# Performance work log

Hardware: AMD Instinct MI355X
Metric: run time of the kernel (lower is better)

The kernel has to match this reference:

```python
import jax, jax.numpy as jnp
import numpy as np

N_NODES = 100000
N_EDGES = 1600000
D_IN = 64
D_HID = 64
D_OUT = 64


def setup_inputs() -> dict:
    key = jax.random.key(0)
    ks = jax.random.split(key, 12)
    x = jax.random.normal(ks[0], (N_NODES, D_IN), dtype=jnp.float32)
    edge_index = jax.random.randint(ks[1], (2, N_EDGES), 0, N_NODES, dtype=jnp.int64)
    batch = jnp.zeros((N_NODES,), dtype=jnp.int64)
    # Glorot-ish init for GCNConv weights; PyG stores weight as [in, out] applied as x @ W.
    def lin(k, din, dout):
        s = 1.0 / np.sqrt(din)
        return jax.random.uniform(k, (din, dout), minval=-s, maxval=s, dtype=jnp.float32)
    W1 = lin(ks[2], D_IN, D_HID);  b1 = jnp.zeros((D_HID,), jnp.float32)
    W2 = lin(ks[3], D_HID, D_HID); b2 = jnp.zeros((D_HID,), jnp.float32)
    W3 = lin(ks[4], D_HID, D_HID); b3 = jnp.zeros((D_HID,), jnp.float32)
    W4 = lin(ks[5], D_HID, D_OUT); b4 = jnp.zeros((D_OUT,), jnp.float32)
    return {"x": x, "edge_index": edge_index, "batch": batch,
            "W1": W1, "b1": b1, "W2": W2, "b2": b2,
            "W3": W3, "b3": b3, "W4": W4, "b4": b4}


def reference(x, edge_index, batch, W1, b1, W2, b2, W3, b3, W4, b4):
    N = x.shape[0]
    loops = jnp.arange(N, dtype=edge_index.dtype)
    src = jnp.concatenate([edge_index[0], loops])  # [E+N]
    dst = jnp.concatenate([edge_index[1], loops])  # [E+N]
    # Symmetric normalization: deg over A + I (in-degree at dst), norm_e = d_src^-1/2 * d_dst^-1/2
    deg = jax.ops.segment_sum(jnp.ones(src.shape, dtype=x.dtype), dst, num_segments=N)
    dis = jnp.where(deg > 0, jax.lax.rsqrt(deg), 0.0)
    norm = (dis[src] * dis[dst])[:, None]  # [E+N, 1]

    def conv(h, W, b):
        h = h @ W                                   # [N, dout]
        msg = h[src] * norm                         # gather + scale, [E+N, dout]
        return jax.ops.segment_sum(msg, dst, num_segments=N) + b

    h = jax.nn.elu(conv(x, W1, b1))   # dropout_p=0.0 -> identity
    h = jax.nn.elu(conv(h, W2, b2))
    h = jax.nn.elu(conv(h, W3, b3))
    return conv(h, W4, b4)
```

## Files before the change

### kernel.cpp

```cpp
#include <hip/hip_runtime.h>

#define NN 100000
#define NE 1600000
#define DD 64
#define BSH 9
#define BSZ 512
#define NBKT 196
#define CHUNK 8192
#define NCH ((NE + CHUNK - 1) / CHUNK)
#define CSR2_CAP (NE + 16 * (NBKT * BSZ))


__global__ __launch_bounds__(256) void k_bcount(const int* __restrict__ ei,
                                                int* __restrict__ bcnt) {
    __shared__ int h[NBKT];
    int t = threadIdx.x;
    for (int i = t; i < NBKT; i += 256) h[i] = 0;
    __syncthreads();
    int base = blockIdx.x * CHUNK;
    for (int i = t; i < CHUNK; i += 256) {
        int e = base + i;
        if (e < NE) atomicAdd(&h[ei[NE + e] >> BSH], 1);
    }
    __syncthreads();
    for (int i = t; i < NBKT; i += 256)
        if (h[i]) atomicAdd(&bcnt[i], h[i]);
}


__global__ __launch_bounds__(256) void k_bscan(const int* __restrict__ bcnt,
                                               int* __restrict__ bbase,
                                               int* __restrict__ bcur) {
    __shared__ int s[256];
    int t = threadIdx.x;
    int v = (t < NBKT) ? bcnt[t] : 0;
    s[t] = v;
    __syncthreads();
    for (int o = 1; o < 256; o <<= 1) {
        int x = (t >= o) ? s[t - o] : 0;
        __syncthreads();
        s[t] += x;
        __syncthreads();
    }
    int ex = s[t] - v;
    if (t < NBKT) { bbase[t] = ex; bcur[t] = ex; }
    if (t == NBKT) bbase[NBKT] = ex;
}


__global__ __launch_bounds__(256) void k_bscat(const int* __restrict__ ei,
                                               int* __restrict__ bcur,
                                               int* __restrict__ bkt) {
    __shared__ int h[NBKT], rbase[NBKT], rcur[NBKT];
    int t = threadIdx.x;
    for (int i = t; i < NBKT; i += 256) h[i] = 0;
    __syncthreads();
    int cb = blockIdx.x * CHUNK;
    int s[32], d[32];
#pragma unroll
    for (int i = 0; i < 32; ++i) {
        int e = cb + t + 256 * i;
        if (e < NE) {
            s[i] = ei[e];
            d[i] = ei[NE + e];
            atomicAdd(&h[d[i] >> BSH], 1);
        } else {
            d[i] = -1;
        }
    }
    __syncthreads();
    for (int i = t; i < NBKT; i += 256) {
        int c = h[i];
        rbase[i] = c ? atomicAdd(&bcur[i], c) : 0;
        rcur[i] = 0;
    }
    __syncthreads();
#pragma unroll
    for (int i = 0; i < 32; ++i) {
        if (d[i] >= 0) {
            int b = d[i] >> BSH;
            int pos = rbase[b] + atomicAdd(&rcur[b], 1);
            bkt[pos] = s[i] | ((d[i] & (BSZ - 1)) << 17);
        }
    }
}


__global__ __launch_bounds__(256) void k_ncnt(const int* __restrict__ bbase,
                                              const int* __restrict__ bkt,
                                              int* __restrict__ ncnt,
                                              int* __restrict__ bptot,
                                              double* __restrict__ dis) {
    __shared__ int cnt[BSZ];
    __shared__ int red[256];
    int b = blockIdx.x, t = threadIdx.x;
    cnt[t] = 0; cnt[t + 256] = 0;
    __syncthreads();
    int beg = bbase[b], end = bbase[b + 1];
    for (int j = beg + t; j < end; j += 256)
        atomicAdd(&cnt[bkt[j] >> 17], 1);
    __syncthreads();
    int nb = b * BSZ;
    int n0 = nb + t, n1 = nb + t + 256;
    int c0 = cnt[t], c1 = cnt[t + 256];
    int p0 = (n0 < NN) ? ((c0 + 16) & ~15) : 0;
    int p1 = (n1 < NN) ? ((c1 + 16) & ~15) : 0;
    if (n0 < NN) { ncnt[n0] = c0; dis[n0] = 1.0 / sqrt((double)(c0 + 1)); }
    if (n1 < NN) { ncnt[n1] = c1; dis[n1] = 1.0 / sqrt((double)(c1 + 1)); }
    red[t] = p0 + p1;
    __syncthreads();
    for (int o = 128; o > 0; o >>= 1) {
        if (t < o) red[t] += red[t + o];
        __syncthreads();
    }
    if (t == 0) bptot[b] = red[0];
}


__global__ __launch_bounds__(256) void k_pscan(const int* __restrict__ bptot,
                                               int* __restrict__ pbase,
                                               int* __restrict__ rp2) {
    __shared__ int s[256];
    int t = threadIdx.x;
    int v = (t < NBKT) ? bptot[t] : 0;
    s[t] = v;
    __syncthreads();
    for (int o = 1; o < 256; o <<= 1) {
        int x = (t >= o) ? s[t - o] : 0;
        __syncthreads();
        s[t] += x;
        __syncthreads();
    }
    int ex = s[t] - v;
    if (t < NBKT) pbase[t] = ex;
    if (t == NBKT) rp2[NN] = ex;
}


__global__ __launch_bounds__(256) void k_bfill(const int* __restrict__ bbase,
                                               const int* __restrict__ bkt,
                                               const int* __restrict__ ncnt,
                                               const int* __restrict__ pbase,
                                               int* __restrict__ rp2,
                                               int* __restrict__ csr2) {
    __shared__ int cur[BSZ];
    __shared__ int s2[256];
    int b = blockIdx.x, t = threadIdx.x;
    int nb = b * BSZ;
    int gbase = pbase[b];
    int n0 = nb + 2 * t, n1 = nb + 2 * t + 1;
    int c0 = (n0 < NN) ? ncnt[n0] : -1;
    int c1 = (n1 < NN) ? ncnt[n1] : -1;
    int q0 = (c0 >= 0) ? ((c0 + 16) & ~15) : 0;
    int q1 = (c1 >= 0) ? ((c1 + 16) & ~15) : 0;
    s2[t] = q0 + q1;
    __syncthreads();
    for (int o = 1; o < 256; o <<= 1) {
        int v = (t >= o) ? s2[t - o] : 0;
        __syncthreads();
        s2[t] += v;
        __syncthreads();
    }
    int ex = s2[t] - (q0 + q1);
    if (c0 >= 0) { int g = gbase + ex;      rp2[n0] = g; csr2[g] = n0; cur[2 * t]     = ex + 1; }
    if (c1 >= 0) { int g = gbase + ex + q0; rp2[n1] = g; csr2[g] = n1; cur[2 * t + 1] = ex + q0 + 1; }
    __syncthreads();
    int beg = bbase[b], end = bbase[b + 1];
    for (int j = beg + t; j < end; j += 256) {
        int pk = bkt[j];
        int pos = gbase + atomicAdd(&cur[pk >> 17], 1);
        csr2[pos] = pk & 0x1FFFF;
    }
    __syncthreads();
    if (c0 >= 0) { int e0 = ex + q0;      for (int j = cur[2 * t];     j < e0; ++j) csr2[gbase + j] = NN; }
    if (c1 >= 0) { int e1 = ex + q0 + q1; for (int j = cur[2 * t + 1]; j < e1; ++j) csr2[gbase + j] = NN; }
}


__global__ __launch_bounds__(256) void k_gemm(const float* __restrict__ in,
                                              const float* __restrict__ W,
                                              const double* __restrict__ dis,
                                              float* __restrict__ h2s) {
    __shared__ float sW[DD * DD];
    __shared__ float sIn[128 * 65];
    int t = threadIdx.x;
    int brow = blockIdx.x * 128;
#pragma unroll
    for (int i = 0; i < 16; ++i) sW[t + 256 * i] = W[t + 256 * i];
#pragma unroll
    for (int i = 0; i < 32; ++i) {
        int idx = t + 256 * i;
        int rr = idx >> 6, kk = idx & 63;
        int gr = brow + rr; if (gr >= NN) gr = NN - 1;
        sIn[rr * 65 + kk] = in[(size_t)gr * DD + kk];
    }
    __syncthreads();
    int cg = t & 7;
    int rg = t >> 3;
    const float* sInB = &sIn[rg * 4 * 65];

    float aE[4][8], aO[4][8];
#pragma unroll
    for (int i = 0; i < 4; ++i)
#pragma unroll
        for (int j = 0; j < 8; ++j) { aE[i][j] = 0.f; aO[i][j] = 0.f; }

#pragma unroll 4
    for (int k = 0; k < DD; k += 2) {
        float4 w0 = *(const float4*)&sW[k * DD + cg * 8];
        float4 w1 = *(const float4*)&sW[k * DD + cg * 8 + 4];
        float4 w2 = *(const float4*)&sW[(k + 1) * DD + cg * 8];
        float4 w3 = *(const float4*)&sW[(k + 1) * DD + cg * 8 + 4];
        float wv0[8] = {w0.x, w0.y, w0.z, w0.w, w1.x, w1.y, w1.z, w1.w};
        float wv1[8] = {w2.x, w2.y, w2.z, w2.w, w3.x, w3.y, w3.z, w3.w};
#pragma unroll
        for (int i = 0; i < 4; ++i) {
            float a0 = sInB[i * 65 + k];
            float a1 = sInB[i * 65 + k + 1];
#pragma unroll
            for (int j = 0; j < 8; ++j) {
                aE[i][j] = fmaf(a0, wv0[j], aE[i][j]);
                aO[i][j] = fmaf(a1, wv1[j], aO[i][j]);
            }
        }
    }

#pragma unroll
    for (int i = 0; i < 4; ++i) {
        int row = brow + rg * 4 + i;
        if (row < NN) {
            double dr = dis[row];
            float o[8];
#pragma unroll
            for (int j = 0; j < 8; ++j)
                o[j] = (float)((double)(aE[i][j] + aO[i][j]) * dr);
            *(float4*)&h2s[(size_t)row * DD + cg * 8]     = make_float4(o[0], o[1], o[2], o[3]);
            *(float4*)&h2s[(size_t)row * DD + cg * 8 + 4] = make_float4(o[4], o[5], o[6], o[7]);
        }
    }
}


__global__ __launch_bounds__(256) void k_aggr(const int* __restrict__ rp2,
                                              const int* __restrict__ csr2,
                                              const float* __restrict__ h2s,
                                              const double* __restrict__ dis,
                                              const float* __restrict__ b,
                                              float* __restrict__ out,
                                              int apply_elu) {
    int gid = blockIdx.x * 256 + threadIdx.x;
    int node = gid >> 6;
    int lane = gid & 63;
    int beg = __builtin_amdgcn_readfirstlane(rp2[node]);
    int end = __builtin_amdgcn_readfirstlane(rp2[node + 1]);
    double a0 = 0.0, a1 = 0.0, a2 = 0.0, a3 = 0.0;
    for (int j = beg; j < end; j += 16) {
        int4 i0 = *(const int4*)&csr2[j];
        int4 i1 = *(const int4*)&csr2[j + 4];
        int4 i2 = *(const int4*)&csr2[j + 8];
        int4 i3 = *(const int4*)&csr2[j + 12];
        float v0  = h2s[(size_t)(unsigned)i0.x * DD + lane];
        float v1  = h2s[(size_t)(unsigned)i0.y * DD + lane];
        float v2  = h2s[(size_t)(unsigned)i0.z * DD + lane];
        float v3  = h2s[(size_t)(unsigned)i0.w * DD + lane];
        float v4  = h2s[(size_t)(unsigned)i1.x * DD + lane];
        float v5  = h2s[(size_t)(unsigned)i1.y * DD + lane];
        float v6  = h2s[(size_t)(unsigned)i1.z * DD + lane];
        float v7  = h2s[(size_t)(unsigned)i1.w * DD + lane];
        float v8  = h2s[(size_t)(unsigned)i2.x * DD + lane];
        float v9  = h2s[(size_t)(unsigned)i2.y * DD + lane];
        float v10 = h2s[(size_t)(unsigned)i2.z * DD + lane];
        float v11 = h2s[(size_t)(unsigned)i2.w * DD + lane];
        float v12 = h2s[(size_t)(unsigned)i3.x * DD + lane];
        float v13 = h2s[(size_t)(unsigned)i3.y * DD + lane];
        float v14 = h2s[(size_t)(unsigned)i3.z * DD + lane];
        float v15 = h2s[(size_t)(unsigned)i3.w * DD + lane];
        a0 += (double)v0;  a1 += (double)v1;  a2 += (double)v2;  a3 += (double)v3;
        a0 += (double)v4;  a1 += (double)v5;  a2 += (double)v6;  a3 += (double)v7;
        a0 += (double)v8;  a1 += (double)v9;  a2 += (double)v10; a3 += (double)v11;
        a0 += (double)v12; a1 += (double)v13; a2 += (double)v14; a3 += (double)v15;
    }
    double sum = (a0 + a1) + (a2 + a3);
    float vf = (float)(dis[node] * sum + (double)b[lane]);
    if (apply_elu && vf <= 0.f) vf = expm1f(vf);
    out[gid] = vf;
}


static inline size_t align256(size_t x) { return (x + 255) & ~(size_t)255; }

extern "C" void kernel_launch(void* const* d_in, const int* in_sizes, int n_in,
                              void* d_out, int out_size, void* d_ws, size_t ws_size,
                              hipStream_t stream) {
    const float* x  = (const float*)d_in[0];
    const int*   ei = (const int*)d_in[1];
    const float* W1 = (const float*)d_in[3];
    const float* b1 = (const float*)d_in[4];
    const float* W2 = (const float*)d_in[5];
    const float* b2 = (const float*)d_in[6];
    const float* W3 = (const float*)d_in[7];
    const float* b3 = (const float*)d_in[8];
    const float* W4 = (const float*)d_in[9];
    const float* b4 = (const float*)d_in[10];
    float* out = (float*)d_out;

    char* ws = (char*)d_ws;
    size_t off = 0;
    double* dis   = (double*)(ws + off); off = align256(off + (size_t)NN * sizeof(double));
    float*  h2s   = (float*) (ws + off); off = align256(off + (size_t)(NN + 1) * DD * sizeof(float));
    float*  A     = (float*) (ws + off); off = align256(off + (size_t)NN * DD * sizeof(float));
    int*    ncnt  = (int*)   (ws + off); off = align256(off + (size_t)NN * sizeof(int));
    int*    rp2   = (int*)   (ws + off); off = align256(off + (size_t)(NN + 1) * sizeof(int));
    int*    bcnt  = (int*)   (ws + off); off = align256(off + (size_t)(NBKT + 1) * sizeof(int));
    int*    bbase = (int*)   (ws + off); off = align256(off + (size_t)(NBKT + 1) * sizeof(int));
    int*    bcur  = (int*)   (ws + off); off = align256(off + (size_t)(NBKT + 1) * sizeof(int));
    int*    bptot = (int*)   (ws + off); off = align256(off + (size_t)(NBKT + 1) * sizeof(int));
    int*    pbase = (int*)   (ws + off); off = align256(off + (size_t)(NBKT + 1) * sizeof(int));
    int*    bkt   = (int*)   (ws + off); off = align256(off + (size_t)NE * sizeof(int));
    int*    csr2  = (int*)   (ws + off); off = align256(off + (size_t)CSR2_CAP * sizeof(int));

    hipMemsetAsync(bcnt, 0, (size_t)NBKT * sizeof(int), stream);
    hipMemsetAsync(h2s + (size_t)NN * DD, 0, DD * sizeof(float), stream);

    k_bcount<<<NCH, 256, 0, stream>>>(ei, bcnt);
    k_bscan<<<1, 256, 0, stream>>>(bcnt, bbase, bcur);
    k_bscat<<<NCH, 256, 0, stream>>>(ei, bcur, bkt);
    k_ncnt<<<NBKT, 256, 0, stream>>>(bbase, bkt, ncnt, bptot, dis);
    k_pscan<<<1, 256, 0, stream>>>(bptot, pbase, rp2);
    k_bfill<<<NBKT, 256, 0, stream>>>(bbase, bkt, ncnt, pbase, rp2, csr2);

    struct Layer { const float* in; const float* b; const float* W; float* o; int elu; };
    Layer L[4] = {
        { x,   b1, W1, A,   1 },
        { A,   b2, W2, out, 1 },
        { out, b3, W3, A,   1 },
        { A,   b4, W4, out, 0 },
    };

    for (int l = 0; l < 4; ++l) {
        k_gemm<<<(NN + 127) / 128, 256, 0, stream>>>(L[l].in, L[l].W, dis, h2s);
        k_aggr<<<NN / 4, 256, 0, stream>>>(rp2, csr2, h2s, dis, L[l].b, L[l].o, L[l].elu);
    }
}
```

Baseline: 386.9 us.

## Fuse aggregation with next-layer GEMM and streamline CSR build with fixed-capacity buckets

The CSR construction drops the counting pass and the two scan kernels. Edges are scattered into fixed-capacity per-bucket arrays, and one merge kernel counts, pads, computes the degree norms and fills the CSR, taking its global offset from an atomic counter. For layers 1-3, a new persistent-wave kernel fuses neighbour aggregation, bias, ELU and the next layer's 64x64 matmul, broadcasting values with readlane. This removes the intermediate activation round trip through memory and three GEMM launches. The costs are 64 weight registers per lane, serial readlane matmul work, a capacity assumption on bucket size (BCAP) that could overflow, and a less regular, atomic-dependent CSR order.

```diff
diff --git a/kernel.cpp b/kernel.cpp
--- a/kernel.cpp
+++ b/kernel.cpp
@@ -6,45 +6,19 @@
 #define BSH 9
 #define BSZ 512
 #define NBKT 196
+#define BCAP 16384
 #define CHUNK 8192
 #define NCH ((NE + CHUNK - 1) / CHUNK)
-#define CSR2_CAP (NE + 16 * (NBKT * BSZ))
-
-
-__global__ __launch_bounds__(256) void k_bcount(const int* __restrict__ ei,
-                                                int* __restrict__ bcnt) {
-    __shared__ int h[NBKT];
+#define CSR2_CAP (NE + 16 * NN + 1024)
+
+
+__global__ void k_zero(int* __restrict__ bcur, int* __restrict__ gcur,
+                       float* __restrict__ h2sA, float* __restrict__ h2sB) {
     int t = threadIdx.x;
-    for (int i = t; i < NBKT; i += 256) h[i] = 0;
-    __syncthreads();
-    int base = blockIdx.x * CHUNK;
-    for (int i = t; i < CHUNK; i += 256) {
-        int e = base + i;
-        if (e < NE) atomicAdd(&h[ei[NE + e] >> BSH], 1);
-    }
-    __syncthreads();
-    for (int i = t; i < NBKT; i += 256)
-        if (h[i]) atomicAdd(&bcnt[i], h[i]);
-}
-
-
-__global__ __launch_bounds__(256) void k_bscan(const int* __restrict__ bcnt,
-                                               int* __restrict__ bbase,
-                                               int* __restrict__ bcur) {
-    __shared__ int s[256];
-    int t = threadIdx.x;
-    int v = (t < NBKT) ? bcnt[t] : 0;
-    s[t] = v;
-    __syncthreads();
-    for (int o = 1; o < 256; o <<= 1) {
-        int x = (t >= o) ? s[t - o] : 0;
-        __syncthreads();
-        s[t] += x;
-        __syncthreads();
-    }
-    int ex = s[t] - v;
-    if (t < NBKT) { bbase[t] = ex; bcur[t] = ex; }
-    if (t == NBKT) bbase[NBKT] = ex;
+    if (t < NBKT) bcur[t] = 0;
+    if (t == 255) *gcur = 0;
+    if (t < DD) h2sA[(size_t)NN * DD + t] = 0.f;
+    if (t >= 64 && t < 128) h2sB[(size_t)NN * DD + (t - 64)] = 0.f;
 }
 
 
@@ -80,77 +54,35 @@
         if (d[i] >= 0) {
             int b = d[i] >> BSH;
             int pos = rbase[b] + atomicAdd(&rcur[b], 1);
-            bkt[pos] = s[i] | ((d[i] & (BSZ - 1)) << 17);
-        }
-    }
-}
-
-
-__global__ __launch_bounds__(256) void k_ncnt(const int* __restrict__ bbase,
-                                              const int* __restrict__ bkt,
-                                              int* __restrict__ ncnt,
-                                              int* __restrict__ bptot,
-                                              double* __restrict__ dis) {
+            bkt[(size_t)b * BCAP + pos] = s[i] | ((d[i] & (BSZ - 1)) << 17);
+        }
+    }
+}
+
+
+__global__ __launch_bounds__(256) void k_merge(const int* __restrict__ bcur,
+                                               const int* __restrict__ bkt,
+                                               int* __restrict__ gcur,
+                                               int* __restrict__ rbeg,
+                                               int* __restrict__ rlen,
+                                               double* __restrict__ dis,
+                                               int* __restrict__ csr2) {
     __shared__ int cnt[BSZ];
-    __shared__ int red[256];
+    __shared__ int cur[BSZ];
+    __shared__ int s2[256];
+    __shared__ int sbase;
     int b = blockIdx.x, t = threadIdx.x;
     cnt[t] = 0; cnt[t + 256] = 0;
     __syncthreads();
-    int beg = bbase[b], end = bbase[b + 1];
-    for (int j = beg + t; j < end; j += 256)
-        atomicAdd(&cnt[bkt[j] >> 17], 1);
+    int ec = bcur[b];
+    const int* row = bkt + (size_t)b * BCAP;
+    for (int j = t; j < ec; j += 256)
+        atomicAdd(&cnt[row[j] >> 17], 1);
     __syncthreads();
     int nb = b * BSZ;
-    int n0 = nb + t, n1 = nb + t + 256;
-    int c0 = cnt[t], c1 = cnt[t + 256];
-    int p0 = (n0 < NN) ? ((c0 + 16) & ~15) : 0;
-    int p1 = (n1 < NN) ? ((c1 + 16) & ~15) : 0;
-    if (n0 < NN) { ncnt[n0] = c0; dis[n0] = 1.0 / sqrt((double)(c0 + 1)); }
-    if (n1 < NN) { ncnt[n1] = c1; dis[n1] = 1.0 / sqrt((double)(c1 + 1)); }
-    red[t] = p0 + p1;
-    __syncthreads();
-    for (int o = 128; o > 0; o >>= 1) {
-        if (t < o) red[t] += red[t + o];
-        __syncthreads();
-    }
-    if (t == 0) bptot[b] = red[0];
-}
-
-
-__global__ __launch_bounds__(256) void k_pscan(const int* __restrict__ bptot,
-                                               int* __restrict__ pbase,
-                                               int* __restrict__ rp2) {
-    __shared__ int s[256];
-    int t = threadIdx.x;
-    int v = (t < NBKT) ? bptot[t] : 0;
-    s[t] = v;
-    __syncthreads();
-    for (int o = 1; o < 256; o <<= 1) {
-        int x = (t >= o) ? s[t - o] : 0;
-        __syncthreads();
-        s[t] += x;
-        __syncthreads();
-    }
-    int ex = s[t] - v;
-    if (t < NBKT) pbase[t] = ex;
-    if (t == NBKT) rp2[NN] = ex;
-}
-
-
-__global__ __launch_bounds__(256) void k_bfill(const int* __restrict__ bbase,
-                                               const int* __restrict__ bkt,
-                                               const int* __restrict__ ncnt,
-                                               const int* __restrict__ pbase,
-                                               int* __restrict__ rp2,
-                                               int* __restrict__ csr2) {
-    __shared__ int cur[BSZ];
-    __shared__ int s2[256];
-    int b = blockIdx.x, t = threadIdx.x;
-    int nb = b * BSZ;
-    int gbase = pbase[b];
     int n0 = nb + 2 * t, n1 = nb + 2 * t + 1;
-    int c0 = (n0 < NN) ? ncnt[n0] : -1;
-    int c1 = (n1 < NN) ? ncnt[n1] : -1;
+    int c0 = (n0 < NN) ? cnt[2 * t] : -1;
+    int c1 = (n1 < NN) ? cnt[2 * t + 1] : -1;
     int q0 = (c0 >= 0) ? ((c0 + 16) & ~15) : 0;
     int q1 = (c1 >= 0) ? ((c1 + 16) & ~15) : 0;
     s2[t] = q0 + q1;
@@ -161,19 +93,31 @@
         s2[t] += v;
         __syncthreads();
     }
+    if (t == 255) sbase = atomicAdd(gcur, s2[255]);
+    __syncthreads();
+    int base = sbase;
     int ex = s2[t] - (q0 + q1);
-    if (c0 >= 0) { int g = gbase + ex;      rp2[n0] = g; csr2[g] = n0; cur[2 * t]     = ex + 1; }
-    if (c1 >= 0) { int g = gbase + ex + q0; rp2[n1] = g; csr2[g] = n1; cur[2 * t + 1] = ex + q0 + 1; }
-    __syncthreads();
-    int beg = bbase[b], end = bbase[b + 1];
-    for (int j = beg + t; j < end; j += 256) {
-        int pk = bkt[j];
-        int pos = gbase + atomicAdd(&cur[pk >> 17], 1);
+    if (c0 >= 0) {
+        rbeg[n0] = base + ex; rlen[n0] = q0;
+        dis[n0] = 1.0 / sqrt((double)(c0 + 1));
+        csr2[base + ex] = n0;
+        cur[2 * t] = ex + 1;
+    }
+    if (c1 >= 0) {
+        rbeg[n1] = base + ex + q0; rlen[n1] = q1;
+        dis[n1] = 1.0 / sqrt((double)(c1 + 1));
+        csr2[base + ex + q0] = n1;
+        cur[2 * t + 1] = ex + q0 + 1;
+    }
+    __syncthreads();
+    for (int j = t; j < ec; j += 256) {
+        int pk = row[j];
+        int pos = base + atomicAdd(&cur[pk >> 17], 1);
         csr2[pos] = pk & 0x1FFFF;
     }
     __syncthreads();
-    if (c0 >= 0) { int e0 = ex + q0;      for (int j = cur[2 * t];     j < e0; ++j) csr2[gbase + j] = NN; }
-    if (c1 >= 0) { int e1 = ex + q0 + q1; for (int j = cur[2 * t + 1]; j < e1; ++j) csr2[gbase + j] = NN; }
+    if (c0 >= 0) { int e0 = ex + q0;      for (int j = cur[2 * t];     j < e0; ++j) csr2[base + j] = NN; }
+    if (c1 >= 0) { int e1 = ex + q0 + q1; for (int j = cur[2 * t + 1]; j < e1; ++j) csr2[base + j] = NN; }
 }
 
 
@@ -241,18 +185,71 @@
 }
 
 
-__global__ __launch_bounds__(256) void k_aggr(const int* __restrict__ rp2,
+__global__ __launch_bounds__(256) void k_fag(const int* __restrict__ rbeg,
+                                             const int* __restrict__ rlen,
+                                             const int* __restrict__ csr2,
+                                             const float* __restrict__ h2s_old,
+                                             const double* __restrict__ dis,
+                                             const float* __restrict__ bias,
+                                             const float* __restrict__ W,
+                                             float* __restrict__ h2s_new) {
+    int t = threadIdx.x;
+    int lane = t & 63;
+    float wk[64];
+#pragma unroll
+    for (int k = 0; k < 64; ++k) wk[k] = W[k * DD + lane];
+    float bv = bias[lane];
+    int wglob = blockIdx.x * 4 + (t >> 6);
+    int nwaves = gridDim.x * 4;
+    for (int node = wglob; node < NN; node += nwaves) {
+        int beg = __builtin_amdgcn_readfirstlane(rbeg[node]);
+        int end = beg + __builtin_amdgcn_readfirstlane(rlen[node]);
+        double a0 = 0.0, a1 = 0.0, a2 = 0.0, a3 = 0.0;
+        for (int j = beg; j < end; j += 8) {
+            int4 i0 = *(const int4*)&csr2[j];
+            int4 i1 = *(const int4*)&csr2[j + 4];
+            float v0 = h2s_old[(size_t)(unsigned)i0.x * DD + lane];
+            float v1 = h2s_old[(size_t)(unsigned)i0.y * DD + lane];
+            float v2 = h2s_old[(size_t)(unsigned)i0.z * DD + lane];
+            float v3 = h2s_old[(size_t)(unsigned)i0.w * DD + lane];
+            float v4 = h2s_old[(size_t)(unsigned)i1.x * DD + lane];
+            float v5 = h2s_old[(size_t)(unsigned)i1.y * DD + lane];
+            float v6 = h2s_old[(size_t)(unsigned)i1.z * DD + lane];
+            float v7 = h2s_old[(size_t)(unsigned)i1.w * DD + lane];
+            a0 += (double)v0; a1 += (double)v1;
+            a2 += (double)v2; a3 += (double)v3;
+            a0 += (double)v4; a1 += (double)v5;
+            a2 += (double)v6; a3 += (double)v7;
+        }
+        double dn = dis[node];
+        float vf = (float)(dn * ((a0 + a1) + (a2 + a3)) + (double)bv);
+        if (vf <= 0.f) vf = expm1f(vf);
+        int vb = __float_as_int(vf);
+        float accE = 0.f, accO = 0.f;
+#pragma unroll
+        for (int k = 0; k < 64; k += 2) {
+            float h0 = __int_as_float(__builtin_amdgcn_readlane(vb, k));
+            float h1 = __int_as_float(__builtin_amdgcn_readlane(vb, k + 1));
+            accE = fmaf(h0, wk[k], accE);
+            accO = fmaf(h1, wk[k + 1], accO);
+        }
+        h2s_new[(size_t)node * DD + lane] = (float)((double)(accE + accO) * dn);
+    }
+}
+
+
+__global__ __launch_bounds__(256) void k_aggr(const int* __restrict__ rbeg,
+                                              const int* __restrict__ rlen,
                                               const int* __restrict__ csr2,
                                               const float* __restrict__ h2s,
                                               const double* __restrict__ dis,
                                               const float* __restrict__ b,
-                                              float* __restrict__ out,
-                                              int apply_elu) {
+                                              float* __restrict__ out) {
     int gid = blockIdx.x * 256 + threadIdx.x;
     int node = gid >> 6;
     int lane = gid & 63;
-    int beg = __builtin_amdgcn_readfirstlane(rp2[node]);
-    int end = __builtin_amdgcn_readfirstlane(rp2[node + 1]);
+    int beg = __builtin_amdgcn_readfirstlane(rbeg[node]);
+    int end = beg + __builtin_amdgcn_readfirstlane(rlen[node]);
     double a0 = 0.0, a1 = 0.0, a2 = 0.0, a3 = 0.0;
     for (int j = beg; j < end; j += 16) {
         int4 i0 = *(const int4*)&csr2[j];
@@ -281,9 +278,7 @@
         a0 += (double)v12; a1 += (double)v13; a2 += (double)v14; a3 += (double)v15;
     }
     double sum = (a0 + a1) + (a2 + a3);
-    float vf = (float)(dis[node] * sum + (double)b[lane]);
-    if (apply_elu && vf <= 0.f) vf = expm1f(vf);
-    out[gid] = vf;
+    out[gid] = (float)(dis[node] * sum + (double)b[lane]);
 }
 
 
@@ -306,39 +301,24 @@
 
     char* ws = (char*)d_ws;
     size_t off = 0;
-    double* dis   = (double*)(ws + off); off = align256(off + (size_t)NN * sizeof(double));
-    float*  h2s   = (float*) (ws + off); off = align256(off + (size_t)(NN + 1) * DD * sizeof(float));
-    float*  A     = (float*) (ws + off); off = align256(off + (size_t)NN * DD * sizeof(float));
-    int*    ncnt  = (int*)   (ws + off); off = align256(off + (size_t)NN * sizeof(int));
-    int*    rp2   = (int*)   (ws + off); off = align256(off + (size_t)(NN + 1) * sizeof(int));
-    int*    bcnt  = (int*)   (ws + off); off = align256(off + (size_t)(NBKT + 1) * sizeof(int));
-    int*    bbase = (int*)   (ws + off); off = align256(off + (size_t)(NBKT + 1) * sizeof(int));
-    int*    bcur  = (int*)   (ws + off); off = align256(off + (size_t)(NBKT + 1) * sizeof(int));
-    int*    bptot = (int*)   (ws + off); off = align256(off + (size_t)(NBKT + 1) * sizeof(int));
-    int*    pbase = (int*)   (ws + off); off = align256(off + (size_t)(NBKT + 1) * sizeof(int));
-    int*    bkt   = (int*)   (ws + off); off = align256(off + (size_t)NE * sizeof(int));
-    int*    csr2  = (int*)   (ws + off); off = align256(off + (size_t)CSR2_CAP * sizeof(int));
-
-    hipMemsetAsync(bcnt, 0, (size_t)NBKT * sizeof(int), stream);
-    hipMemsetAsync(h2s + (size_t)NN * DD, 0, DD * sizeof(float), stream);
-
-    k_bcount<<<NCH, 256, 0, stream>>>(ei, bcnt);
-    k_bscan<<<1, 256, 0, stream>>>(bcnt, bbase, bcur);
+    float*  h2sA = (float*) (ws + off); off = align256(off + (size_t)(NN + 1) * DD * sizeof(float));
+    float*  h2sB = (float*) (ws + off); off = align256(off + (size_t)(NN + 1) * DD * sizeof(float));
+    double* dis  = (double*)(ws + off); off = align256(off + (size_t)NN * sizeof(double));
+    int*    rbeg = (int*)   (ws + off); off = align256(off + (size_t)NN * sizeof(int));
+    int*    rlen = (int*)   (ws + off); off = align256(off + (size_t)NN * sizeof(int));
+    int*    bcur = (int*)   (ws + off); off = align256(off + (size_t)(NBKT + 1) * sizeof(int));
+    int*    gcur = (int*)   (ws + off); off = align256(off + 256 * sizeof(int));
+    int*    bkt  = (int*)   (ws + off); off = align256(off + (size_t)NBKT * BCAP * sizeof(int));
+    int*    csr2 = (int*)   (ws + off); off = align256(off + (size_t)CSR2_CAP * sizeof(int));
+
+    k_zero <<<1, 256, 0, stream>>>(bcur, gcur, h2sA, h2sB);
     k_bscat<<<NCH, 256, 0, stream>>>(ei, bcur, bkt);
-    k_ncnt<<<NBKT, 256, 0, stream>>>(bbase, bkt, ncnt, bptot, dis);
-    k_pscan<<<1, 256, 0, stream>>>(bptot, pbase, rp2);
-    k_bfill<<<NBKT, 256, 0, stream>>>(bbase, bkt, ncnt, pbase, rp2, csr2);
-
-    struct Layer { const float* in; const float* b; const float* W; float* o; int elu; };
-    Layer L[4] = {
-        { x,   b1, W1, A,   1 },
-        { A,   b2, W2, out, 1 },
-        { out, b3, W3, A,   1 },
-        { A,   b4, W4, out, 0 },
-    };
-
-    for (int l = 0; l < 4; ++l) {
-        k_gemm<<<(NN + 127) / 128, 256, 0, stream>>>(L[l].in, L[l].W, dis, h2s);
-        k_aggr<<<NN / 4, 256, 0, stream>>>(rp2, csr2, h2s, dis, L[l].b, L[l].o, L[l].elu);
-    }
-}
+    k_merge<<<NBKT, 256, 0, stream>>>(bcur, bkt, gcur, rbeg, rlen, dis, csr2);
+
+    const int NGB = (NN + 127) / 128;
+    k_gemm<<<NGB, 256, 0, stream>>>(x, W1, dis, h2sA);
+    k_fag <<<2048, 256, 0, stream>>>(rbeg, rlen, csr2, h2sA, dis, b1, W2, h2sB);
+    k_fag <<<2048, 256, 0, stream>>>(rbeg, rlen, csr2, h2sB, dis, b2, W3, h2sA);
+    k_fag <<<2048, 256, 0, stream>>>(rbeg, rlen, csr2, h2sA, dis, b3, W4, h2sB);
+    k_aggr<<<NN / 4, 256, 0, stream>>>(rbeg, rlen, csr2, h2sB, dis, b4, out);
+}
```

Result: faster. 378.2 us (-2.3%).
